# Optimization experiments

Measured on AMD Instinct MI355X. Metric: run time of the kernel, lower is better.

## Reference

```python
import jax, jax.numpy as jnp
import numpy as np

NUM_HEADS = 32
NUM_KV_HEADS = 8
HEAD_DIM = 128
SCALE = 0.08838834764831845  # 1/sqrt(HEAD_DIM)
SEQ_LEN = 2048
NEG_INF = -1e30


def setup_inputs() -> dict:
    key = jax.random.key(0)
    k1, k2, k3 = jax.random.split(key, 3)
    query = jax.random.normal(k1, (SEQ_LEN, NUM_HEADS * HEAD_DIM), dtype=jnp.float32)
    key_t = jax.random.normal(k2, (SEQ_LEN, NUM_KV_HEADS * HEAD_DIM), dtype=jnp.float32)
    value = jax.random.normal(k3, (SEQ_LEN, NUM_KV_HEADS * HEAD_DIM), dtype=jnp.float32)
    return {"query": query, "key": key_t, "value": value}


def reference(query, key, value):
    S = query.shape[0]
    n_rep = NUM_HEADS // NUM_KV_HEADS
    # GQA: group q heads by kv head instead of materializing repeated K/V.
    q = query.reshape(S, NUM_KV_HEADS, n_rep, HEAD_DIM)   # [S, G, R, D]
    k = key.reshape(S, NUM_KV_HEADS, HEAD_DIM)            # [S, G, D]
    v = value.reshape(S, NUM_KV_HEADS, HEAD_DIM)          # [S, G, D]
    # scores: [G, R, S(query), S(key)]
    scores = jnp.einsum('sgrd,tgd->grst', q, k) * jnp.float32(SCALE)
    # causal mask (prefill: seq_len > 1 -> is_causal=True)
    causal = jnp.arange(S)[:, None] >= jnp.arange(S)[None, :]  # [S, S]
    scores = jnp.where(causal, scores, NEG_INF)
    probs = jax.nn.softmax(scores, axis=-1)
    out = jnp.einsum('grst,tgd->sgrd', probs, v)          # [S, G, R, D]
    return out.reshape(S, NUM_HEADS * HEAD_DIM)
```

## Files before the change

### kernel.cpp

```cpp
#include <hip/hip_runtime.h>


#define SEQ    2048
#define NH     32
#define NKV    8
#define DHEAD  128
#define QROW   (NH * DHEAD)
#define KVROW  (NKV * DHEAD)
#define SCALE  0.08838834764831845f
#define LOG2E  1.4426950408889634f
#define BM     32
#define BN     64
#define PSTR   72
#define VSTR   132

typedef __attribute__((ext_vector_type(8))) short bf16x8;
typedef __attribute__((ext_vector_type(8))) unsigned short u16x8;
typedef __attribute__((ext_vector_type(4))) float f32x4;

static __device__ __forceinline__ unsigned short f2bf(float f) {
  unsigned int u = __float_as_uint(f);
  return (unsigned short)((u + 0x7fffu + ((u >> 16) & 1u)) >> 16);
}
static __device__ __forceinline__ unsigned short f2bf_fast(float f) {
  return (unsigned short)((__float_as_uint(f) + 0x8000u) >> 16);
}

#define DPP_F(x, ctrl) \
  __int_as_float(__builtin_amdgcn_mov_dpp(__float_as_int(x), (ctrl), 0xf, 0xf, true))
static __device__ __forceinline__ float red16_sum(float x) {
  x += DPP_F(x, 0xB1);
  x += DPP_F(x, 0x4E);
  x += DPP_F(x, 0x141);
  x += DPP_F(x, 0x140);
  return x;
}

__global__ __launch_bounds__(256) void prep_kernel(
    const float* __restrict__ K, const float* __restrict__ V,
    unsigned short* __restrict__ Kg, unsigned short* __restrict__ VTg) {
  __shared__ unsigned short Vs[64 * VSTR];
  const int t0  = blockIdx.x * 64;
  const int g   = blockIdx.y;
  const int tid = threadIdx.x;
  for (int e = 0; e < 8; ++e) {
    int fi = e * 256 + tid;
    int t  = fi >> 5;
    int c4 = fi & 31;
    const float4 kv = *(const float4*)(K + (size_t)(t0 + t) * KVROW + g * DHEAD + c4 * 4);
    ushort4 kb = {f2bf(kv.x), f2bf(kv.y), f2bf(kv.z), f2bf(kv.w)};
    *(ushort4*)(Kg + ((size_t)(g * SEQ + t0 + t) << 7) + c4 * 4) = kb;
    const float4 vv = *(const float4*)(V + (size_t)(t0 + t) * KVROW + g * DHEAD + c4 * 4);
    ushort4 vb = {f2bf(vv.x), f2bf(vv.y), f2bf(vv.z), f2bf(vv.w)};
    *(ushort4*)&Vs[t * VSTR + c4 * 4] = vb;
  }
  __syncthreads();
  for (int e = 0; e < 4; ++e) {
    int idx = e * 256 + tid;
    int d  = idx >> 3;
    int tb = idx & 7;
    u16x8 o;
    for (int j = 0; j < 8; ++j) o[j] = Vs[(tb * 8 + j) * VSTR + d];
    *(u16x8*)(VTg + (size_t)(g * DHEAD + d) * SEQ + t0 + tb * 8) = o;
  }
}

static __device__ __forceinline__ void stage_tile(
    const unsigned short* __restrict__ Kg, const unsigned short* __restrict__ VTg,
    unsigned short* kbuf, unsigned short* vbuf, int g, int kt, int w, int lane) {
  const int t0 = kt * BN;
  for (int c = 0; c < 4; ++c) {
    int off = (w * 4 + c) * 512 + lane * 8;
    int tl  = off >> 7;
    int dsw = (off & 127) ^ (8 * (tl & 7));
    const unsigned short* src = Kg + ((size_t)(g * SEQ + t0 + tl) << 7) + dsw;
    __builtin_amdgcn_global_load_lds(
        (const __attribute__((address_space(1))) void*)src,
        (__attribute__((address_space(3))) void*)(kbuf + (w * 4 + c) * 512), 16, 0, 0);
  }
  for (int c = 0; c < 4; ++c) {
    int off = (w * 4 + c) * 512 + lane * 8;
    int dl  = off >> 6;
    int tsw = (off & 63) ^ (8 * (dl & 7));
    const unsigned short* src = VTg + (size_t)(g * DHEAD + dl) * SEQ + t0 + tsw;
    __builtin_amdgcn_global_load_lds(
        (const __attribute__((address_space(1))) void*)src,
        (__attribute__((address_space(3))) void*)(vbuf + (w * 4 + c) * 512), 16, 0, 0);
  }
}

__global__ __launch_bounds__(256, 2) void sdpa_fa5_kernel(
    const float* __restrict__ Q, float* __restrict__ O,
    const unsigned short* __restrict__ Kg, const unsigned short* __restrict__ VTg) {
  __shared__ unsigned short Kb[2][BN * DHEAD];
  __shared__ unsigned short Vb[2][DHEAD * BN];
  __shared__ unsigned short Ps[4][16 * PSTR];

  const int b  = blockIdx.x;
  const int g  = b & 7;
  const int q5 = (b >> 3) & 31;
  const int jj = (b >= 256) ? q5 : 63 - q5;
  const int q0   = jj * BM;
  const int nt   = (jj >> 1) + 1;
  const int tid  = threadIdx.x;
  const int w    = tid >> 6;
  const int lane = tid & 63;
  const int quad = lane >> 4;
  const int l16  = lane & 15;
  const int h    = g * 4 + w;
  const int sw   = 8 * (l16 & 7);

  bf16x8 qf[2][4];
  for (int mt = 0; mt < 2; ++mt) {
    const float* qrow = Q + (size_t)(q0 + mt * 16 + l16) * QROW + h * DHEAD;
    for (int kc = 0; kc < 4; ++kc) {
      const float* p = qrow + kc * 32 + quad * 8;
      bf16x8 v;
      for (int j = 0; j < 8; ++j) v[j] = (short)f2bf(p[j] * (SCALE * LOG2E));
      qf[mt][kc] = v;
    }
  }

  f32x4 oacc[2][8];
  for (int mt = 0; mt < 2; ++mt)
    for (int i = 0; i < 8; ++i) oacc[mt][i] = (f32x4){0.f, 0.f, 0.f, 0.f};
  float lsum[2][4];
  for (int mt = 0; mt < 2; ++mt)
    for (int r = 0; r < 4; ++r) lsum[mt][r] = 0.f;

  stage_tile(Kg, VTg, Kb[0], Vb[0], g, 0, w, lane);
  __syncthreads();

  for (int kt = 0; kt < nt; ++kt) {
    const int cur = kt & 1;
    if (kt + 1 < nt)
      stage_tile(Kg, VTg, Kb[cur ^ 1], Vb[cur ^ 1], g, kt + 1, w, lane);

    f32x4 sacc[2][4];
    for (int mt = 0; mt < 2; ++mt)
      for (int nb = 0; nb < 4; ++nb) sacc[mt][nb] = (f32x4){0.f, 0.f, 0.f, 0.f};
    for (int nb = 0; nb < 4; ++nb)
      for (int kc = 0; kc < 4; ++kc) {
        bf16x8 kf = *(const bf16x8*)&Kb[cur][(nb * 16 + l16) * DHEAD + ((kc * 32 + quad * 8) ^ sw)];
        sacc[0][nb] = __builtin_amdgcn_mfma_f32_16x16x32_bf16(qf[0][kc], kf, sacc[0][nb], 0, 0, 0);
        sacc[1][nb] = __builtin_amdgcn_mfma_f32_16x16x32_bf16(qf[1][kc], kf, sacc[1][nb], 0, 0, 0);
      }

    bf16x8 pa[2][2];
    const bool diag = (kt == nt - 1);
    for (int mt = 0; mt < 2; ++mt) {
      float pv[4][4];
      for (int nb = 0; nb < 4; ++nb)
        for (int r = 0; r < 4; ++r) {
          float x = sacc[mt][nb][r];
          if (diag) {
            int tg = kt * BN + nb * 16 + l16;
            int rg = q0 + mt * 16 + quad * 4 + r;
            x = (tg > rg) ? -1e30f : x;
          }
          float pe = exp2f(x);
          pv[nb][r] = pe;
        }
      for (int r = 0; r < 4; ++r)
        lsum[mt][r] += (pv[0][r] + pv[1][r]) + (pv[2][r] + pv[3][r]);

      unsigned short* pw = &Ps[w][0];
      for (int nb = 0; nb < 4; ++nb)
        for (int r = 0; r < 4; ++r)
          pw[(quad * 4 + r) * PSTR + nb * 16 + l16] = f2bf_fast(pv[nb][r]);
      for (int kc = 0; kc < 2; ++kc)
        pa[mt][kc] = *(const bf16x8*)&pw[l16 * PSTR + kc * 32 + quad * 8];
    }

    for (int nb2 = 0; nb2 < 8; ++nb2)
      for (int kc = 0; kc < 2; ++kc) {
        bf16x8 vf = *(const bf16x8*)&Vb[cur][(nb2 * 16 + l16) * BN + ((kc * 32 + quad * 8) ^ sw)];
        oacc[0][nb2] = __builtin_amdgcn_mfma_f32_16x16x32_bf16(pa[0][kc], vf, oacc[0][nb2], 0, 0, 0);
        oacc[1][nb2] = __builtin_amdgcn_mfma_f32_16x16x32_bf16(pa[1][kc], vf, oacc[1][nb2], 0, 0, 0);
      }
    __syncthreads();
  }

  for (int mt = 0; mt < 2; ++mt)
    for (int r = 0; r < 4; ++r) {
      float inv = 1.f / red16_sum(lsum[mt][r]);
      float* orow = O + (size_t)(q0 + mt * 16 + quad * 4 + r) * QROW + h * DHEAD;
      for (int nb2 = 0; nb2 < 8; ++nb2)
        orow[nb2 * 16 + l16] = oacc[mt][nb2][r] * inv;
    }
}

extern "C" void kernel_launch(void* const* d_in, const int* in_sizes, int n_in,
                              void* d_out, int out_size, void* d_ws, size_t ws_size,
                              hipStream_t stream) {
  (void)in_sizes; (void)n_in; (void)out_size; (void)ws_size;
  const float* Q = (const float*)d_in[0];
  const float* K = (const float*)d_in[1];
  const float* V = (const float*)d_in[2];
  float* O = (float*)d_out;
  unsigned short* Kg  = (unsigned short*)d_ws;
  unsigned short* VTg = Kg + (size_t)NKV * SEQ * DHEAD;
  prep_kernel<<<dim3(SEQ / 64, NKV), 256, 0, stream>>>(K, V, Kg, VTg);
  sdpa_fa5_kernel<<<512, 256, 0, stream>>>(Q, O, Kg, VTg);
}
```

Baseline: 162.5 us.

## Load K/V MFMA fragments directly from global memory, dropping LDS staging and barriers

Removes the double-buffered LDS staging of K and V tiles and the per-iteration block barrier. Each wave now reads its K and V^T MFMA fragments straight from global memory (relying on L1/L2 for reuse across the four waves sharing a KV head). It also swaps exp2f for the hardware exp2 builtin and widens the P scratch stride. The change gives up explicit async prefetch and shared reuse, so every wave issues its own global loads with exposed latency. In exchange it frees LDS, which may allow higher occupancy.

```diff
diff --git a/kernel.cpp b/kernel.cpp
--- a/kernel.cpp
+++ b/kernel.cpp
@@ -11,8 +11,8 @@
 #define LOG2E  1.4426950408889634f
 #define BM     32
 #define BN     64
-#define PSTR   72
-#define VSTR   132
+#define PSTR   88
+#define VSTRP  132
 
 typedef __attribute__((ext_vector_type(8))) short bf16x8;
 typedef __attribute__((ext_vector_type(8))) unsigned short u16x8;
@@ -39,7 +39,7 @@
 __global__ __launch_bounds__(256) void prep_kernel(
     const float* __restrict__ K, const float* __restrict__ V,
     unsigned short* __restrict__ Kg, unsigned short* __restrict__ VTg) {
-  __shared__ unsigned short Vs[64 * VSTR];
+  __shared__ unsigned short Vs[64 * VSTRP];
   const int t0  = blockIdx.x * 64;
   const int g   = blockIdx.y;
   const int tid = threadIdx.x;
@@ -52,7 +52,7 @@
     *(ushort4*)(Kg + ((size_t)(g * SEQ + t0 + t) << 7) + c4 * 4) = kb;
     const float4 vv = *(const float4*)(V + (size_t)(t0 + t) * KVROW + g * DHEAD + c4 * 4);
     ushort4 vb = {f2bf(vv.x), f2bf(vv.y), f2bf(vv.z), f2bf(vv.w)};
-    *(ushort4*)&Vs[t * VSTR + c4 * 4] = vb;
+    *(ushort4*)&Vs[t * VSTRP + c4 * 4] = vb;
   }
   __syncthreads();
   for (int e = 0; e < 4; ++e) {
@@ -60,40 +60,14 @@
     int d  = idx >> 3;
     int tb = idx & 7;
     u16x8 o;
-    for (int j = 0; j < 8; ++j) o[j] = Vs[(tb * 8 + j) * VSTR + d];
+    for (int j = 0; j < 8; ++j) o[j] = Vs[(tb * 8 + j) * VSTRP + d];
     *(u16x8*)(VTg + (size_t)(g * DHEAD + d) * SEQ + t0 + tb * 8) = o;
   }
 }
 
-static __device__ __forceinline__ void stage_tile(
-    const unsigned short* __restrict__ Kg, const unsigned short* __restrict__ VTg,
-    unsigned short* kbuf, unsigned short* vbuf, int g, int kt, int w, int lane) {
-  const int t0 = kt * BN;
-  for (int c = 0; c < 4; ++c) {
-    int off = (w * 4 + c) * 512 + lane * 8;
-    int tl  = off >> 7;
-    int dsw = (off & 127) ^ (8 * (tl & 7));
-    const unsigned short* src = Kg + ((size_t)(g * SEQ + t0 + tl) << 7) + dsw;
-    __builtin_amdgcn_global_load_lds(
-        (const __attribute__((address_space(1))) void*)src,
-        (__attribute__((address_space(3))) void*)(kbuf + (w * 4 + c) * 512), 16, 0, 0);
-  }
-  for (int c = 0; c < 4; ++c) {
-    int off = (w * 4 + c) * 512 + lane * 8;
-    int dl  = off >> 6;
-    int tsw = (off & 63) ^ (8 * (dl & 7));
-    const unsigned short* src = VTg + (size_t)(g * DHEAD + dl) * SEQ + t0 + tsw;
-    __builtin_amdgcn_global_load_lds(
-        (const __attribute__((address_space(1))) void*)src,
-        (__attribute__((address_space(3))) void*)(vbuf + (w * 4 + c) * 512), 16, 0, 0);
-  }
-}
-
-__global__ __launch_bounds__(256, 2) void sdpa_fa5_kernel(
+__global__ __launch_bounds__(256, 2) void sdpa_fa6_kernel(
     const float* __restrict__ Q, float* __restrict__ O,
     const unsigned short* __restrict__ Kg, const unsigned short* __restrict__ VTg) {
-  __shared__ unsigned short Kb[2][BN * DHEAD];
-  __shared__ unsigned short Vb[2][DHEAD * BN];
   __shared__ unsigned short Ps[4][16 * PSTR];
 
   const int b  = blockIdx.x;
@@ -108,7 +82,6 @@
   const int quad = lane >> 4;
   const int l16  = lane & 15;
   const int h    = g * 4 + w;
-  const int sw   = 8 * (l16 & 7);
 
   bf16x8 qf[2][4];
   for (int mt = 0; mt < 2; ++mt) {
@@ -128,23 +101,36 @@
   for (int mt = 0; mt < 2; ++mt)
     for (int r = 0; r < 4; ++r) lsum[mt][r] = 0.f;
 
-  stage_tile(Kg, VTg, Kb[0], Vb[0], g, 0, w, lane);
-  __syncthreads();
+  const unsigned short* kbase = Kg + (((size_t)g * SEQ + l16) << 7) + quad * 8;
+  const unsigned short* vbase = VTg + ((size_t)g * DHEAD + l16) * SEQ + quad * 8;
+  unsigned short* pw = &Ps[w][0];
 
   for (int kt = 0; kt < nt; ++kt) {
-    const int cur = kt & 1;
-    if (kt + 1 < nt)
-      stage_tile(Kg, VTg, Kb[cur ^ 1], Vb[cur ^ 1], g, kt + 1, w, lane);
+    const unsigned short* kp = kbase + ((size_t)kt * BN << 7);
+    const unsigned short* vp = vbase + (size_t)kt * BN;
 
     f32x4 sacc[2][4];
     for (int mt = 0; mt < 2; ++mt)
       for (int nb = 0; nb < 4; ++nb) sacc[mt][nb] = (f32x4){0.f, 0.f, 0.f, 0.f};
-    for (int nb = 0; nb < 4; ++nb)
-      for (int kc = 0; kc < 4; ++kc) {
-        bf16x8 kf = *(const bf16x8*)&Kb[cur][(nb * 16 + l16) * DHEAD + ((kc * 32 + quad * 8) ^ sw)];
-        sacc[0][nb] = __builtin_amdgcn_mfma_f32_16x16x32_bf16(qf[0][kc], kf, sacc[0][nb], 0, 0, 0);
-        sacc[1][nb] = __builtin_amdgcn_mfma_f32_16x16x32_bf16(qf[1][kc], kf, sacc[1][nb], 0, 0, 0);
-      }
+    for (int nb = 0; nb < 4; ++nb) {
+      bf16x8 kf0 = *(const bf16x8*)(kp + ((size_t)nb * 16 << 7) + 0 * 32);
+      bf16x8 kf1 = *(const bf16x8*)(kp + ((size_t)nb * 16 << 7) + 1 * 32);
+      bf16x8 kf2 = *(const bf16x8*)(kp + ((size_t)nb * 16 << 7) + 2 * 32);
+      bf16x8 kf3 = *(const bf16x8*)(kp + ((size_t)nb * 16 << 7) + 3 * 32);
+      sacc[0][nb] = __builtin_amdgcn_mfma_f32_16x16x32_bf16(qf[0][0], kf0, sacc[0][nb], 0, 0, 0);
+      sacc[1][nb] = __builtin_amdgcn_mfma_f32_16x16x32_bf16(qf[1][0], kf0, sacc[1][nb], 0, 0, 0);
+      sacc[0][nb] = __builtin_amdgcn_mfma_f32_16x16x32_bf16(qf[0][1], kf1, sacc[0][nb], 0, 0, 0);
+      sacc[1][nb] = __builtin_amdgcn_mfma_f32_16x16x32_bf16(qf[1][1], kf1, sacc[1][nb], 0, 0, 0);
+      sacc[0][nb] = __builtin_amdgcn_mfma_f32_16x16x32_bf16(qf[0][2], kf2, sacc[0][nb], 0, 0, 0);
+      sacc[1][nb] = __builtin_amdgcn_mfma_f32_16x16x32_bf16(qf[1][2], kf2, sacc[1][nb], 0, 0, 0);
+      sacc[0][nb] = __builtin_amdgcn_mfma_f32_16x16x32_bf16(qf[0][3], kf3, sacc[0][nb], 0, 0, 0);
+      sacc[1][nb] = __builtin_amdgcn_mfma_f32_16x16x32_bf16(qf[1][3], kf3, sacc[1][nb], 0, 0, 0);
+    }
+
+    bf16x8 vfr[8][2];
+    for (int nb2 = 0; nb2 < 8; ++nb2)
+      for (int kc = 0; kc < 2; ++kc)
+        vfr[nb2][kc] = *(const bf16x8*)(vp + (size_t)(nb2 * 16) * SEQ + kc * 32);
 
     bf16x8 pa[2][2];
     const bool diag = (kt == nt - 1);
@@ -158,13 +144,10 @@
             int rg = q0 + mt * 16 + quad * 4 + r;
             x = (tg > rg) ? -1e30f : x;
           }
-          float pe = exp2f(x);
-          pv[nb][r] = pe;
+          pv[nb][r] = __builtin_amdgcn_exp2f(x);
         }
       for (int r = 0; r < 4; ++r)
         lsum[mt][r] += (pv[0][r] + pv[1][r]) + (pv[2][r] + pv[3][r]);
-
-      unsigned short* pw = &Ps[w][0];
       for (int nb = 0; nb < 4; ++nb)
         for (int r = 0; r < 4; ++r)
           pw[(quad * 4 + r) * PSTR + nb * 16 + l16] = f2bf_fast(pv[nb][r]);
@@ -174,11 +157,9 @@
 
     for (int nb2 = 0; nb2 < 8; ++nb2)
       for (int kc = 0; kc < 2; ++kc) {
-        bf16x8 vf = *(const bf16x8*)&Vb[cur][(nb2 * 16 + l16) * BN + ((kc * 32 + quad * 8) ^ sw)];
-        oacc[0][nb2] = __builtin_amdgcn_mfma_f32_16x16x32_bf16(pa[0][kc], vf, oacc[0][nb2], 0, 0, 0);
-        oacc[1][nb2] = __builtin_amdgcn_mfma_f32_16x16x32_bf16(pa[1][kc], vf, oacc[1][nb2], 0, 0, 0);
+        oacc[0][nb2] = __builtin_amdgcn_mfma_f32_16x16x32_bf16(pa[0][kc], vfr[nb2][kc], oacc[0][nb2], 0, 0, 0);
+        oacc[1][nb2] = __builtin_amdgcn_mfma_f32_16x16x32_bf16(pa[1][kc], vfr[nb2][kc], oacc[1][nb2], 0, 0, 0);
       }
-    __syncthreads();
   }
 
   for (int mt = 0; mt < 2; ++mt)
@@ -201,5 +182,5 @@
   unsigned short* Kg  = (unsigned short*)d_ws;
   unsigned short* VTg = Kg + (size_t)NKV * SEQ * DHEAD;
   prep_kernel<<<dim3(SEQ / 64, NKV), 256, 0, stream>>>(K, V, Kg, VTg);
-  sdpa_fa5_kernel<<<512, 256, 0, stream>>>(Q, O, Kg, VTg);
+  sdpa_fa6_kernel<<<512, 256, 0, stream>>>(Q, O, Kg, VTg);
 }
```

Measured after the change: 212.6 us. 30.8% more time.

## Halve query tile, read V directly from global, skip masked diagonal work

Applied to the files above, without the earlier changes.

Query rows per block drop from 32 to 16, so the grid grows to 1024 blocks with occupancy raised to 4 blocks per CU, and a new scheduling map balances causal work. V fragments are no longer staged in LDS; they are loaded straight from global into registers and split into two halves to overlap with the QK MFMAs. The diagonal tile is peeled out and only computes the unmasked key sub-blocks, and the P scratch buffer uses an XOR swizzle instead of padding. The trade-off is that K/V reuse per block drops by half and V global reads become uncoalesced 16-byte row fragments.

```diff
diff --git a/kernel.cpp b/kernel.cpp
--- a/kernel.cpp
+++ b/kernel.cpp
@@ -9,10 +9,8 @@
 #define KVROW  (NKV * DHEAD)
 #define SCALE  0.08838834764831845f
 #define LOG2E  1.4426950408889634f
-#define BM     32
 #define BN     64
-#define PSTR   72
-#define VSTR   132
+#define VSTRP  132
 
 typedef __attribute__((ext_vector_type(8))) short bf16x8;
 typedef __attribute__((ext_vector_type(8))) unsigned short u16x8;
@@ -39,7 +37,7 @@
 __global__ __launch_bounds__(256) void prep_kernel(
     const float* __restrict__ K, const float* __restrict__ V,
     unsigned short* __restrict__ Kg, unsigned short* __restrict__ VTg) {
-  __shared__ unsigned short Vs[64 * VSTR];
+  __shared__ unsigned short Vs[64 * VSTRP];
   const int t0  = blockIdx.x * 64;
   const int g   = blockIdx.y;
   const int tid = threadIdx.x;
@@ -52,7 +50,7 @@
     *(ushort4*)(Kg + ((size_t)(g * SEQ + t0 + t) << 7) + c4 * 4) = kb;
     const float4 vv = *(const float4*)(V + (size_t)(t0 + t) * KVROW + g * DHEAD + c4 * 4);
     ushort4 vb = {f2bf(vv.x), f2bf(vv.y), f2bf(vv.z), f2bf(vv.w)};
-    *(ushort4*)&Vs[t * VSTR + c4 * 4] = vb;
+    *(ushort4*)&Vs[t * VSTRP + c4 * 4] = vb;
   }
   __syncthreads();
   for (int e = 0; e < 4; ++e) {
@@ -60,14 +58,14 @@
     int d  = idx >> 3;
     int tb = idx & 7;
     u16x8 o;
-    for (int j = 0; j < 8; ++j) o[j] = Vs[(tb * 8 + j) * VSTR + d];
+    for (int j = 0; j < 8; ++j) o[j] = Vs[(tb * 8 + j) * VSTRP + d];
     *(u16x8*)(VTg + (size_t)(g * DHEAD + d) * SEQ + t0 + tb * 8) = o;
   }
 }
 
-static __device__ __forceinline__ void stage_tile(
-    const unsigned short* __restrict__ Kg, const unsigned short* __restrict__ VTg,
-    unsigned short* kbuf, unsigned short* vbuf, int g, int kt, int w, int lane) {
+static __device__ __forceinline__ void stage_k(
+    const unsigned short* __restrict__ Kg, unsigned short* kbuf,
+    int g, int kt, int w, int lane) {
   const int t0 = kt * BN;
   for (int c = 0; c < 4; ++c) {
     int off = (w * 4 + c) * 512 + lane * 8;
@@ -78,30 +76,22 @@
         (const __attribute__((address_space(1))) void*)src,
         (__attribute__((address_space(3))) void*)(kbuf + (w * 4 + c) * 512), 16, 0, 0);
   }
-  for (int c = 0; c < 4; ++c) {
-    int off = (w * 4 + c) * 512 + lane * 8;
-    int dl  = off >> 6;
-    int tsw = (off & 63) ^ (8 * (dl & 7));
-    const unsigned short* src = VTg + (size_t)(g * DHEAD + dl) * SEQ + t0 + tsw;
-    __builtin_amdgcn_global_load_lds(
-        (const __attribute__((address_space(1))) void*)src,
-        (__attribute__((address_space(3))) void*)(vbuf + (w * 4 + c) * 512), 16, 0, 0);
-  }
-}
-
-__global__ __launch_bounds__(256, 2) void sdpa_fa5_kernel(
+}
+
+__global__ __launch_bounds__(256, 4) void sdpa_fa7_kernel(
     const float* __restrict__ Q, float* __restrict__ O,
     const unsigned short* __restrict__ Kg, const unsigned short* __restrict__ VTg) {
   __shared__ unsigned short Kb[2][BN * DHEAD];
-  __shared__ unsigned short Vb[2][DHEAD * BN];
-  __shared__ unsigned short Ps[4][16 * PSTR];
+  __shared__ unsigned short Ps[4][16 * 64];
 
   const int b  = blockIdx.x;
   const int g  = b & 7;
-  const int q5 = (b >> 3) & 31;
-  const int jj = (b >= 256) ? q5 : 63 - q5;
-  const int q0   = jj * BM;
-  const int nt   = (jj >> 1) + 1;
+  const int i  = b >> 3;
+  const int s  = i & 31;
+  const int m  = i >> 5;
+  const int jj = m + 4 * ((m & 1) ? (31 - s) : s);
+  const int q0 = jj * 16;
+  const int nt = (jj >> 2) + 1;
   const int tid  = threadIdx.x;
   const int w    = tid >> 6;
   const int lane = tid & 63;
@@ -110,84 +100,111 @@
   const int h    = g * 4 + w;
   const int sw   = 8 * (l16 & 7);
 
-  bf16x8 qf[2][4];
-  for (int mt = 0; mt < 2; ++mt) {
-    const float* qrow = Q + (size_t)(q0 + mt * 16 + l16) * QROW + h * DHEAD;
+  bf16x8 qf[4];
+  {
+    const float* qrow = Q + (size_t)(q0 + l16) * QROW + h * DHEAD;
     for (int kc = 0; kc < 4; ++kc) {
       const float* p = qrow + kc * 32 + quad * 8;
       bf16x8 v;
       for (int j = 0; j < 8; ++j) v[j] = (short)f2bf(p[j] * (SCALE * LOG2E));
-      qf[mt][kc] = v;
+      qf[kc] = v;
     }
   }
 
-  f32x4 oacc[2][8];
-  for (int mt = 0; mt < 2; ++mt)
-    for (int i = 0; i < 8; ++i) oacc[mt][i] = (f32x4){0.f, 0.f, 0.f, 0.f};
-  float lsum[2][4];
-  for (int mt = 0; mt < 2; ++mt)
-    for (int r = 0; r < 4; ++r) lsum[mt][r] = 0.f;
-
-  stage_tile(Kg, VTg, Kb[0], Vb[0], g, 0, w, lane);
+  f32x4 oacc[8];
+  for (int i2 = 0; i2 < 8; ++i2) oacc[i2] = (f32x4){0.f, 0.f, 0.f, 0.f};
+  float lsum[4] = {0.f, 0.f, 0.f, 0.f};
+
+  const unsigned short* vbase = VTg + ((size_t)g * DHEAD + l16) * SEQ + quad * 8;
+  unsigned short* pw = &Ps[w][0];
+  const int pxq = 32 * (quad & 1);
+
+  stage_k(Kg, Kb[0], g, 0, w, lane);
   __syncthreads();
 
-  for (int kt = 0; kt < nt; ++kt) {
+  for (int kt = 0; kt < nt - 1; ++kt) {
     const int cur = kt & 1;
-    if (kt + 1 < nt)
-      stage_tile(Kg, VTg, Kb[cur ^ 1], Vb[cur ^ 1], g, kt + 1, w, lane);
-
-    f32x4 sacc[2][4];
-    for (int mt = 0; mt < 2; ++mt)
-      for (int nb = 0; nb < 4; ++nb) sacc[mt][nb] = (f32x4){0.f, 0.f, 0.f, 0.f};
-    for (int nb = 0; nb < 4; ++nb)
+    const unsigned short* vp = vbase + (size_t)kt * BN;
+
+    bf16x8 vfa[4][2];
+    for (int nb2 = 0; nb2 < 4; ++nb2)
+      for (int kc = 0; kc < 2; ++kc)
+        vfa[nb2][kc] = *(const bf16x8*)(vp + (size_t)(nb2 * 16) * SEQ + kc * 32);
+
+    stage_k(Kg, Kb[cur ^ 1], g, kt + 1, w, lane);
+
+    for (int nb = 0; nb < 4; ++nb) {
+      f32x4 sacc = (f32x4){0.f, 0.f, 0.f, 0.f};
       for (int kc = 0; kc < 4; ++kc) {
         bf16x8 kf = *(const bf16x8*)&Kb[cur][(nb * 16 + l16) * DHEAD + ((kc * 32 + quad * 8) ^ sw)];
-        sacc[0][nb] = __builtin_amdgcn_mfma_f32_16x16x32_bf16(qf[0][kc], kf, sacc[0][nb], 0, 0, 0);
-        sacc[1][nb] = __builtin_amdgcn_mfma_f32_16x16x32_bf16(qf[1][kc], kf, sacc[1][nb], 0, 0, 0);
-      }
-
-    bf16x8 pa[2][2];
-    const bool diag = (kt == nt - 1);
-    for (int mt = 0; mt < 2; ++mt) {
-      float pv[4][4];
-      for (int nb = 0; nb < 4; ++nb)
-        for (int r = 0; r < 4; ++r) {
-          float x = sacc[mt][nb][r];
-          if (diag) {
-            int tg = kt * BN + nb * 16 + l16;
-            int rg = q0 + mt * 16 + quad * 4 + r;
-            x = (tg > rg) ? -1e30f : x;
-          }
-          float pe = exp2f(x);
-          pv[nb][r] = pe;
-        }
-      for (int r = 0; r < 4; ++r)
-        lsum[mt][r] += (pv[0][r] + pv[1][r]) + (pv[2][r] + pv[3][r]);
-
-      unsigned short* pw = &Ps[w][0];
-      for (int nb = 0; nb < 4; ++nb)
-        for (int r = 0; r < 4; ++r)
-          pw[(quad * 4 + r) * PSTR + nb * 16 + l16] = f2bf_fast(pv[nb][r]);
-      for (int kc = 0; kc < 2; ++kc)
-        pa[mt][kc] = *(const bf16x8*)&pw[l16 * PSTR + kc * 32 + quad * 8];
+        sacc = __builtin_amdgcn_mfma_f32_16x16x32_bf16(qf[kc], kf, sacc, 0, 0, 0);
+      }
+      float psum = 0.f;
+      for (int r = 0; r < 4; ++r) {
+        float p = __builtin_amdgcn_exp2f(sacc[r]);
+        lsum[r] += p;
+        pw[(quad * 4 + r) * 64 + ((nb * 16 + l16) ^ (pxq + 8 * r))] = f2bf_fast(p);
+        (void)psum;
+      }
     }
 
+    bf16x8 pa[2];
+    for (int kc = 0; kc < 2; ++kc)
+      pa[kc] = *(const bf16x8*)&pw[l16 * 64 + ((kc * 32 + quad * 8) ^ sw)];
+
+    bf16x8 vfb[4][2];
+    for (int nb2 = 0; nb2 < 4; ++nb2)
+      for (int kc = 0; kc < 2; ++kc)
+        vfb[nb2][kc] = *(const bf16x8*)(vp + (size_t)((nb2 + 4) * 16) * SEQ + kc * 32);
+
+    for (int nb2 = 0; nb2 < 4; ++nb2)
+      for (int kc = 0; kc < 2; ++kc)
+        oacc[nb2] = __builtin_amdgcn_mfma_f32_16x16x32_bf16(pa[kc], vfa[nb2][kc], oacc[nb2], 0, 0, 0);
+    for (int nb2 = 0; nb2 < 4; ++nb2)
+      for (int kc = 0; kc < 2; ++kc)
+        oacc[nb2 + 4] = __builtin_amdgcn_mfma_f32_16x16x32_bf16(pa[kc], vfb[nb2][kc], oacc[nb2 + 4], 0, 0, 0);
+
+    __syncthreads();
+  }
+
+  {
+    const int kt  = nt - 1;
+    const int cur = kt & 1;
+    const int kcEff = ((jj & 3) >> 1) + 1;
+    const int nbCmp = kcEff * 2;
+    const unsigned short* vp = vbase + (size_t)kt * BN;
+
+    for (int nb = 0; nb < nbCmp; ++nb) {
+      f32x4 sacc = (f32x4){0.f, 0.f, 0.f, 0.f};
+      for (int kc = 0; kc < 4; ++kc) {
+        bf16x8 kf = *(const bf16x8*)&Kb[cur][(nb * 16 + l16) * DHEAD + ((kc * 32 + quad * 8) ^ sw)];
+        sacc = __builtin_amdgcn_mfma_f32_16x16x32_bf16(qf[kc], kf, sacc, 0, 0, 0);
+      }
+      const int tg = kt * BN + nb * 16 + l16;
+      for (int r = 0; r < 4; ++r) {
+        const int rg = q0 + quad * 4 + r;
+        float x = (tg > rg) ? -1e30f : sacc[r];
+        float p = __builtin_amdgcn_exp2f(x);
+        lsum[r] += p;
+        pw[(quad * 4 + r) * 64 + ((nb * 16 + l16) ^ (pxq + 8 * r))] = f2bf_fast(p);
+      }
+    }
+    bf16x8 pa[2];
+    for (int kc = 0; kc < kcEff; ++kc)
+      pa[kc] = *(const bf16x8*)&pw[l16 * 64 + ((kc * 32 + quad * 8) ^ sw)];
     for (int nb2 = 0; nb2 < 8; ++nb2)
-      for (int kc = 0; kc < 2; ++kc) {
-        bf16x8 vf = *(const bf16x8*)&Vb[cur][(nb2 * 16 + l16) * BN + ((kc * 32 + quad * 8) ^ sw)];
-        oacc[0][nb2] = __builtin_amdgcn_mfma_f32_16x16x32_bf16(pa[0][kc], vf, oacc[0][nb2], 0, 0, 0);
-        oacc[1][nb2] = __builtin_amdgcn_mfma_f32_16x16x32_bf16(pa[1][kc], vf, oacc[1][nb2], 0, 0, 0);
-      }
-    __syncthreads();
-  }
-
-  for (int mt = 0; mt < 2; ++mt)
-    for (int r = 0; r < 4; ++r) {
-      float inv = 1.f / red16_sum(lsum[mt][r]);
-      float* orow = O + (size_t)(q0 + mt * 16 + quad * 4 + r) * QROW + h * DHEAD;
-      for (int nb2 = 0; nb2 < 8; ++nb2)
-        orow[nb2 * 16 + l16] = oacc[mt][nb2][r] * inv;
-    }
+      for (int kc = 0; kc < kcEff; ++kc) {
+        bf16x8 vf = *(const bf16x8*)(vp + (size_t)(nb2 * 16) * SEQ + kc * 32);
+        oacc[nb2] = __builtin_amdgcn_mfma_f32_16x16x32_bf16(pa[kc], vf, oacc[nb2], 0, 0, 0);
+      }
+  }
+
+  for (int r = 0; r < 4; ++r) {
+    float inv = 1.f / red16_sum(lsum[r]);
+    float* orow = O + (size_t)(q0 + quad * 4 + r) * QROW + h * DHEAD;
+    for (int nb2 = 0; nb2 < 8; ++nb2)
+      orow[nb2 * 16 + l16] = oacc[nb2][r] * inv;
+  }
 }
 
 extern "C" void kernel_launch(void* const* d_in, const int* in_sizes, int n_in,
@@ -201,5 +218,5 @@
   unsigned short* Kg  = (unsigned short*)d_ws;
   unsigned short* VTg = Kg + (size_t)NKV * SEQ * DHEAD;
   prep_kernel<<<dim3(SEQ / 64, NKV), 256, 0, stream>>>(K, V, Kg, VTg);
-  sdpa_fa5_kernel<<<512, 256, 0, stream>>>(Q, O, Kg, VTg);
-}
+  sdpa_fa7_kernel<<<1024, 256, 0, stream>>>(Q, O, Kg, VTg);
+}
```

New measurement: 259.4 us. 59.6% more time.
